# Kernel optimization log

Hardware: AMD Instinct MI355X
Metric: run time of the kernel (lower is better)

Reference implementation:

```python
import jax, jax.numpy as jnp
import numpy as np

DIM = 128
HEADS = 4
GN_GROUPS = 4
EPS = 1e-5


def setup_inputs() -> dict:
    key = jax.random.key(0)
    ks = jax.random.split(key, 6)
    B, C, H, W = 4, DIM, 64, 64
    x = jax.random.normal(ks[0], (B, C, H, W), dtype=jnp.float32)
    # 1x1 convs are channel matmuls: store as [out_ch, in_ch]
    w_qkv = jax.random.normal(ks[1], (3 * C, C), dtype=jnp.float32) * (C ** -0.5)
    w_out = jax.random.normal(ks[2], (C, C), dtype=jnp.float32) * (C ** -0.5)
    b_out = jax.random.normal(ks[3], (C,), dtype=jnp.float32) * 0.01
    gn_gamma = jnp.ones((C,), dtype=jnp.float32)
    gn_beta = jnp.zeros((C,), dtype=jnp.float32)
    return {"x": x, "w_qkv": w_qkv, "w_out": w_out, "b_out": b_out,
            "gn_gamma": gn_gamma, "gn_beta": gn_beta}


def _attention_block(x, w_qkv, w_out, b_out, gn_gamma, gn_beta):
    b, c, h, w = x.shape
    d = c // HEADS
    scale = d ** -0.5
    # 1x1 conv == per-pixel matmul over channels
    qkv = jnp.einsum('bchw,oc->bohw', x, w_qkv)  # [b, 3c, h, w]
    q, k, v = jnp.split(qkv, 3, axis=1)
    # 'b (h d) x y -> b h (x y) d'
    def to_heads(t):
        return t.reshape(b, HEADS, d, h * w).transpose(0, 1, 3, 2)  # [b, H, N, d]
    q, k, v = to_heads(q), to_heads(k), to_heads(v)
    dots = jnp.einsum('bhnd,bhmd->bhnm', q, k) * scale  # [b, H, N, N]
    attn = jax.nn.softmax(dots, axis=-1)
    out = jnp.einsum('bhnm,bhmd->bhnd', attn, v)  # [b, H, N, d]
    # 'b h (x y) d -> b (h d) x y'
    out = out.transpose(0, 1, 3, 2).reshape(b, c, h, w)
    # output 1x1 conv + bias
    out = jnp.einsum('bchw,oc->bohw', out, w_out) + b_out[None, :, None, None]
    # GroupNorm(4, c)
    g = out.reshape(b, GN_GROUPS, c // GN_GROUPS, h, w)
    mean = g.mean(axis=(2, 3, 4), keepdims=True)
    var = g.var(axis=(2, 3, 4), keepdims=True)
    g = (g - mean) * jax.lax.rsqrt(var + EPS)
    out = g.reshape(b, c, h, w) * gn_gamma[None, :, None, None] + gn_beta[None, :, None, None]
    return out + x


def reference(x, w_qkv, w_out, b_out, gn_gamma, gn_beta):
    return _attention_block(x, w_qkv, w_out, b_out, gn_gamma, gn_beta)
```

## Files before the change

kernel.cpp:

```cpp
#include <hip/hip_runtime.h>

#define DIM   128
#define NPIX  4096
#define DHEAD 32

using u16 = unsigned short;
typedef __attribute__((ext_vector_type(8))) short   short8;
typedef __attribute__((ext_vector_type(8))) u16     ushort8;
typedef __attribute__((ext_vector_type(4))) float   floatx4;
typedef __attribute__((ext_vector_type(2))) unsigned int uint2v;

#define SCL 0.25513899f

__device__ __forceinline__ float bf2f(u16 u) {
  union { unsigned int i; float f; } v; v.i = ((unsigned int)u) << 16; return v.f;
}
__device__ __forceinline__ u16 f2bf(float f) {
  union { unsigned int i; float f; } v; v.f = f;
  unsigned int i = v.i;
  return (u16)((i + 0x7FFFu + ((i >> 16) & 1u)) >> 16);
}
__device__ __forceinline__ unsigned int pk2bf(float a, float b) {
  union { float f; unsigned int u; } ua, ub; ua.f = a; ub.f = b;
  return __builtin_amdgcn_perm(ub.u, ua.u, 0x07060302u);
}

template<bool F32> __device__ __forceinline__ float ld1(const void* p, size_t i) {
  if constexpr (F32) return ((const float*)p)[i];
  else               return bf2f(((const u16*)p)[i]);
}
template<bool F32> __device__ __forceinline__ float4 ld4(const void* p, size_t i) {
  if constexpr (F32) {
    return *(const float4*)((const float*)p + i);
  } else {
    const ushort4 u = *(const ushort4*)((const u16*)p + i);
    return make_float4(bf2f(u.x), bf2f(u.y), bf2f(u.z), bf2f(u.w));
  }
}
template<bool F32> __device__ __forceinline__ void st4(void* p, size_t i, float4 v) {
  if constexpr (F32) {
    *(float4*)((float*)p + i) = v;
  } else {
    ushort4 u; u.x = f2bf(v.x); u.y = f2bf(v.y); u.z = f2bf(v.z); u.w = f2bf(v.w);
    *(ushort4*)((u16*)p + i) = u;
  }
}

__global__ void k_detect(const u16* __restrict__ x, int* __restrict__ flag,
                         float* __restrict__ S) {
  if (threadIdx.x < 40) S[threadIdx.x] = 0.f;
  if (threadIdx.x == 0 && blockIdx.x == 0) {
    int big = 0;
    for (int i = 0; i < 128; ++i) {
      const float v = bf2f(x[i]);
      if (!(fabsf(v) < 1e4f)) big = 1;
    }
    *flag = big;
  }
}

template<bool F32>
__global__ __launch_bounds__(256) void k_qkv(const void* __restrict__ x,
                                             const void* __restrict__ wqkv,
                                             u16* __restrict__ Q,
                                             u16* __restrict__ K,
                                             u16* __restrict__ V,
                                             const int* __restrict__ flag) {
  if (*flag != (F32 ? 1 : 0)) return;
  const int b = blockIdx.z, y = blockIdx.y, pt = blockIdx.x;
  const int tl = threadIdx.x;
  __shared__ float Ws[32 * 129];
  if (y < 8) {
    const int m = y >> 2, h = y & 3;
    const int ddq = tl & 3, pw = tl >> 2;
    const int rb = m * DIM + h * 32;
    for (int i = tl; i < 32 * DIM; i += 256)
      Ws[(i >> 7) * 129 + (i & 127)] =
          ld1<F32>(wqkv, (size_t)(rb + (i >> 7)) * DIM + (i & 127));
    __syncthreads();
    const int p0 = pt * 256 + pw * 4;
    float acc[8][4];
#pragma unroll
    for (int j = 0; j < 8; ++j) { acc[j][0] = acc[j][1] = acc[j][2] = acc[j][3] = 0.f; }
    const size_t xb = (size_t)b * DIM * NPIX + p0;
    for (int c = 0; c < DIM; ++c) {
      const float4 xv = ld4<F32>(x, xb + (size_t)c * NPIX);
#pragma unroll
      for (int j = 0; j < 8; ++j) {
        const float wv = Ws[(ddq * 8 + j) * 129 + c];
        acc[j][0] += wv * xv.x; acc[j][1] += wv * xv.y;
        acc[j][2] += wv * xv.z; acc[j][3] += wv * xv.w;
      }
    }
    u16* dst = (m == 0) ? Q : K;
    const float scl = (m == 0) ? 1.f : SCL;
    const int bh = b * 4 + h;
#pragma unroll
    for (int t = 0; t < 4; ++t) {
      ushort8 w8;
#pragma unroll
      for (int j = 0; j < 8; ++j) w8[j] = f2bf(acc[j][t] * scl);
      *(ushort8*)(dst + ((size_t)bh * NPIX + p0 + t) * DHEAD + ddq * 8) = w8;
    }
  } else {
    const int og = (y - 8) * 4 + (pt >> 2);
    const int ptv = pt & 3;
    for (int i = tl; i < 8 * DIM; i += 256)
      Ws[(i >> 7) * 129 + (i & 127)] =
          ld1<F32>(wqkv, (size_t)(2 * DIM + og * 8 + (i >> 7)) * DIM + (i & 127));
    __syncthreads();
    const int p0 = ptv * 1024 + tl * 4;
    float acc[8][4];
#pragma unroll
    for (int j = 0; j < 8; ++j) { acc[j][0] = acc[j][1] = acc[j][2] = acc[j][3] = 0.f; }
    const size_t xb = (size_t)b * DIM * NPIX + p0;
    for (int c = 0; c < DIM; ++c) {
      const float4 xv = ld4<F32>(x, xb + (size_t)c * NPIX);
#pragma unroll
      for (int j = 0; j < 8; ++j) {
        const float wv = Ws[j * 129 + c];
        acc[j][0] += wv * xv.x; acc[j][1] += wv * xv.y;
        acc[j][2] += wv * xv.z; acc[j][3] += wv * xv.w;
      }
    }
#pragma unroll
    for (int j = 0; j < 8; ++j) {
      const int c = og * 8 + j;
      ushort4 w4;
      w4.x = f2bf(acc[j][0]); w4.y = f2bf(acc[j][1]);
      w4.z = f2bf(acc[j][2]); w4.w = f2bf(acc[j][3]);
      *(ushort4*)(V + ((size_t)b * DIM + c) * NPIX + p0) = w4;
    }
  }
}

__device__ __forceinline__ short8 xform_p(unsigned c0, unsigned c1,
                                          unsigned c2, unsigned c3) {
  uint2v sw = __builtin_amdgcn_permlane32_swap(c0, c2, false, false);
  uint2v sx = __builtin_amdgcn_permlane16_swap(sw[0], sw[1], false, false);
  uint2v sy = __builtin_amdgcn_permlane32_swap(c1, c3, false, false);
  uint2v sz = __builtin_amdgcn_permlane16_swap(sy[0], sy[1], false, false);
  union { unsigned u[4]; short8 s; } r;
  r.u[0] = sx[0]; r.u[1] = sz[0]; r.u[2] = sx[1]; r.u[3] = sz[1];
  return r.s;
}

__global__ __launch_bounds__(256) void k_attn(const u16* __restrict__ Q,
                                              const u16* __restrict__ K,
                                              const u16* __restrict__ V,
                                              u16* __restrict__ O) {
  const int bh = blockIdx.y, qb = blockIdx.x;
  const int tid = threadIdx.x;
  const int wv = tid >> 6, lane = tid & 63;
  const int quad = lane >> 4, l15 = lane & 15;
  const int b = bh >> 2, h = bh & 3;

  __shared__ __align__(16) u16 Klds[2][64 * 40];
  __shared__ __align__(16) u16 Vlds[2][32 * 72];
  __shared__ __align__(16) u16 Olds[32 * 136];

  const int qtok0 = qb * 128 + wv * 32 + l15;
  const short8 qf0 = *(const short8*)(Q + ((size_t)bh * NPIX + qtok0) * DHEAD + quad * 8);
  const short8 qf1 = *(const short8*)(Q + ((size_t)bh * NPIX + qtok0 + 16) * DHEAD + quad * 8);

  floatx4 o00 = {0.f, 0.f, 0.f, 0.f}, o01 = {0.f, 0.f, 0.f, 0.f};
  floatx4 o10 = {0.f, 0.f, 0.f, 0.f}, o11 = {0.f, 0.f, 0.f, 0.f};
  float lp0 = 0.f, lp1 = 0.f;

  const int skey = tid >> 2, sqt = tid & 3;
  const int sdd = tid >> 3, soc = tid & 7;
  const u16* Kg = K + ((size_t)bh * NPIX + skey) * DHEAD + sqt * 8;
  const u16* Vg = V + ((size_t)(b * DIM + h * DHEAD + sdd)) * NPIX + soc * 8;

  {
    const ushort8 k0 = *(const ushort8*)Kg;
    const ushort8 v0 = *(const ushort8*)Vg;
    *(ushort8*)(Klds[0] + skey * 40 + sqt * 8) = k0;
    *(ushort8*)(Vlds[0] + sdd * 72 + soc * 8) = v0;
  }

  for (int ch = 0; ch < 64; ++ch) {
    const int cur = ch & 1, nxt = cur ^ 1;
    __syncthreads();
    ushort8 kpre, vpre;
    if (ch + 1 < 64) {
      kpre = *(const ushort8*)(Kg + (size_t)(ch + 1) * 64 * DHEAD);
      vpre = *(const ushort8*)(Vg + (ch + 1) * 64);
    }
#pragma unroll
    for (int kc = 0; kc < 2; ++kc) {
      unsigned ca[4], cb[4];
#pragma unroll
      for (int s = 0; s < 2; ++s) {
        const int sub = kc * 2 + s;
        const short8 af = *(const short8*)(Klds[cur] + (sub * 16 + l15) * 40 + quad * 8);
        const floatx4 s0 = __builtin_amdgcn_mfma_f32_16x16x32_bf16(
            af, qf0, (floatx4){0.f, 0.f, 0.f, 0.f}, 0, 0, 0);
        const floatx4 s1 = __builtin_amdgcn_mfma_f32_16x16x32_bf16(
            af, qf1, (floatx4){0.f, 0.f, 0.f, 0.f}, 0, 0, 0);
        const float a0 = __builtin_amdgcn_exp2f(s0[0]);
        const float a1 = __builtin_amdgcn_exp2f(s0[1]);
        const float a2 = __builtin_amdgcn_exp2f(s0[2]);
        const float a3 = __builtin_amdgcn_exp2f(s0[3]);
        const float b0 = __builtin_amdgcn_exp2f(s1[0]);
        const float b1 = __builtin_amdgcn_exp2f(s1[1]);
        const float b2 = __builtin_amdgcn_exp2f(s1[2]);
        const float b3 = __builtin_amdgcn_exp2f(s1[3]);
        lp0 += (a0 + a1) + (a2 + a3);
        lp1 += (b0 + b1) + (b2 + b3);
        ca[s * 2 + 0] = pk2bf(a0, a1); ca[s * 2 + 1] = pk2bf(a2, a3);
        cb[s * 2 + 0] = pk2bf(b0, b1); cb[s * 2 + 1] = pk2bf(b2, b3);
      }
      const short8 pa0 = xform_p(ca[0], ca[1], ca[2], ca[3]);
      const short8 pa1 = xform_p(cb[0], cb[1], cb[2], cb[3]);
      const short8 vb0 = *(const short8*)(Vlds[cur] + l15 * 72 + kc * 32 + quad * 8);
      const short8 vb1 = *(const short8*)(Vlds[cur] + (16 + l15) * 72 + kc * 32 + quad * 8);
      o00 = __builtin_amdgcn_mfma_f32_16x16x32_bf16(pa0, vb0, o00, 0, 0, 0);
      o01 = __builtin_amdgcn_mfma_f32_16x16x32_bf16(pa0, vb1, o01, 0, 0, 0);
      o10 = __builtin_amdgcn_mfma_f32_16x16x32_bf16(pa1, vb0, o10, 0, 0, 0);
      o11 = __builtin_amdgcn_mfma_f32_16x16x32_bf16(pa1, vb1, o11, 0, 0, 0);
    }
    if (ch + 1 < 64) {
      *(ushort8*)(Klds[nxt] + skey * 40 + sqt * 8) = kpre;
      *(ushort8*)(Vlds[nxt] + sdd * 72 + soc * 8) = vpre;
    }
  }
  float l0 = lp0, l1 = lp1;
  l0 += __shfl_xor(l0, 16); l0 += __shfl_xor(l0, 32);
  l1 += __shfl_xor(l1, 16); l1 += __shfl_xor(l1, 32);
  float li0[4], li1[4];
#pragma unroll
  for (int r = 0; r < 4; ++r) {
    li0[r] = 1.f / __shfl(l0, (lane & 48) | (quad * 4 + r));
    li1[r] = 1.f / __shfl(l1, (lane & 48) | (quad * 4 + r));
  }
  uint2v w00, w01, w10, w11;
  w00[0] = (unsigned)f2bf(o00[0] * li0[0]) | ((unsigned)f2bf(o00[1] * li0[1]) << 16);
  w00[1] = (unsigned)f2bf(o00[2] * li0[2]) | ((unsigned)f2bf(o00[3] * li0[3]) << 16);
  w01[0] = (unsigned)f2bf(o01[0] * li0[0]) | ((unsigned)f2bf(o01[1] * li0[1]) << 16);
  w01[1] = (unsigned)f2bf(o01[2] * li0[2]) | ((unsigned)f2bf(o01[3] * li0[3]) << 16);
  w10[0] = (unsigned)f2bf(o10[0] * li1[0]) | ((unsigned)f2bf(o10[1] * li1[1]) << 16);
  w10[1] = (unsigned)f2bf(o10[2] * li1[2]) | ((unsigned)f2bf(o10[3] * li1[3]) << 16);
  w11[0] = (unsigned)f2bf(o11[0] * li1[0]) | ((unsigned)f2bf(o11[1] * li1[1]) << 16);
  w11[1] = (unsigned)f2bf(o11[2] * li1[2]) | ((unsigned)f2bf(o11[3] * li1[3]) << 16);
  __syncthreads();
  *(uint2v*)(Olds + l15 * 136 + wv * 32 + quad * 4) = w00;
  *(uint2v*)(Olds + (16 + l15) * 136 + wv * 32 + quad * 4) = w01;
  *(uint2v*)(Olds + l15 * 136 + wv * 32 + 16 + quad * 4) = w10;
  *(uint2v*)(Olds + (16 + l15) * 136 + wv * 32 + 16 + quad * 4) = w11;
  __syncthreads();
  const int d = tid >> 3, oc = tid & 7;
  const u16* orow = Olds + d * 136;
  u16* og = O + ((size_t)(b * DIM + h * DHEAD + d)) * NPIX + qb * 128;
  *(ushort8*)(og + oc * 8)      = *(const ushort8*)(orow + oc * 8);
  *(ushort8*)(og + 64 + oc * 8) = *(const ushort8*)(orow + 64 + oc * 8);
}

template<bool F32>
__global__ __launch_bounds__(256) void k_proj(const u16* __restrict__ O,
                                              const void* __restrict__ wout,
                                              const void* __restrict__ bout,
                                              float* __restrict__ Y,
                                              float* __restrict__ Sred,
                                              const int* __restrict__ flag) {
  if (*flag != (F32 ? 1 : 0)) return;
  const int b = blockIdx.z, og = blockIdx.y, pt = blockIdx.x;
  const int tl = threadIdx.x;
  __shared__ float Ws[8][DIM];
  for (int i = tl; i < 8 * DIM; i += 256)
    Ws[i >> 7][i & 127] = ld1<F32>(wout, (size_t)(og * 8 + (i >> 7)) * DIM + (i & 127));
  __syncthreads();
  const int p0 = pt * 1024 + tl * 4;
  float acc[8][4];
#pragma unroll
  for (int j = 0; j < 8; ++j) { acc[j][0] = acc[j][1] = acc[j][2] = acc[j][3] = 0.f; }
  const u16* Ob = O + (size_t)b * DIM * NPIX + p0;
  for (int c = 0; c < DIM; ++c) {
    const ushort4 xv4 = *(const ushort4*)(Ob + (size_t)c * NPIX);
    const float x0 = bf2f(xv4.x), x1 = bf2f(xv4.y), x2 = bf2f(xv4.z), x3 = bf2f(xv4.w);
#pragma unroll
    for (int j = 0; j < 8; ++j) {
      const float wv = Ws[j][c];
      acc[j][0] += wv * x0; acc[j][1] += wv * x1;
      acc[j][2] += wv * x2; acc[j][3] += wv * x3;
    }
  }
  float s1 = 0.f, s2 = 0.f;
#pragma unroll
  for (int j = 0; j < 8; ++j) {
    const int o = og * 8 + j;
    const float bo = ld1<F32>(bout, o);
    float4 y4;
    y4.x = acc[j][0] + bo; y4.y = acc[j][1] + bo;
    y4.z = acc[j][2] + bo; y4.w = acc[j][3] + bo;
    *(float4*)(Y + ((size_t)b * DIM + o) * NPIX + p0) = y4;
    s1 += y4.x + y4.y + y4.z + y4.w;
    s2 += y4.x * y4.x + y4.y * y4.y + y4.z * y4.z + y4.w * y4.w;
  }
  __shared__ float red[2][256];
  red[0][tl] = s1; red[1][tl] = s2;
  __syncthreads();
  for (int off = 128; off >= 1; off >>= 1) {
    if (tl < off) { red[0][tl] += red[0][tl + off]; red[1][tl] += red[1][tl + off]; }
    __syncthreads();
  }
  if (tl == 0) {
    const int g = og >> 2;
    atomicAdd(&Sred[(b * 4 + g) * 2 + 0], red[0][0]);
    atomicAdd(&Sred[(b * 4 + g) * 2 + 1], red[1][0]);
  }
}

template<bool F32>
__global__ __launch_bounds__(256) void k_gn(const float* __restrict__ Y,
                                            const float* __restrict__ Sred,
                                            const void* __restrict__ x,
                                            const void* __restrict__ gamma,
                                            const void* __restrict__ beta,
                                            void* __restrict__ out,
                                            const int* __restrict__ flag) {
  if (*flag != (F32 ? 1 : 0)) return;
  const int idx = (blockIdx.x * 256 + threadIdx.x) * 4;
  const int b = idx >> 19;
  const int c = (idx >> 12) & 127;
  const int g = c >> 5;
  const float inv_n = 1.f / (32.f * 4096.f);
  const float s1 = Sred[(b * 4 + g) * 2 + 0];
  const float s2 = Sred[(b * 4 + g) * 2 + 1];
  const float mean = s1 * inv_n;
  const float var = s2 * inv_n - mean * mean;
  const float rs = rsqrtf(var + 1e-5f);
  const float ga = ld1<F32>(gamma, c) * rs;
  const float be = ld1<F32>(beta, c) - mean * ga;
  const float4 y4 = *(const float4*)(Y + idx);
  const float4 xv = ld4<F32>(x, idx);
  float4 r;
  r.x = y4.x * ga + be + xv.x;
  r.y = y4.y * ga + be + xv.y;
  r.z = y4.z * ga + be + xv.z;
  r.w = y4.w * ga + be + xv.w;
  st4<F32>(out, idx, r);
}

extern "C" void kernel_launch(void* const* d_in, const int* in_sizes, int n_in,
                              void* d_out, int out_size, void* d_ws, size_t ws_size,
                              hipStream_t stream) {
  const void* x     = d_in[0];
  const void* wqkv  = d_in[1];
  const void* wout  = d_in[2];
  const void* bout  = d_in[3];
  const void* gamma = d_in[4];
  const void* beta  = d_in[5];
  char* ws = (char*)d_ws;
  u16*   Q = (u16*)(ws + ((size_t)0  << 20));
  u16*   K = (u16*)(ws + ((size_t)8  << 20));
  u16*   V = (u16*)(ws + ((size_t)16 << 20));
  u16*   O = (u16*)(ws + ((size_t)24 << 20));
  float* Y = (float*)(ws + ((size_t)32 << 20));
  float* S = (float*)(ws + ((size_t)40 << 20));
  int*   F = (int*)(ws + ((size_t)40 << 20) + 128);

  k_detect<<<1, 64, 0, stream>>>((const u16*)x, F, S);

  k_qkv<false><<<dim3(16, 12, 4), 256, 0, stream>>>(x, wqkv, Q, K, V, F);
  k_qkv<true> <<<dim3(16, 12, 4), 256, 0, stream>>>(x, wqkv, Q, K, V, F);
  k_attn<<<dim3(32, 16), 256, 0, stream>>>(Q, K, V, O);
  k_proj<false><<<dim3(4, 16, 4), 256, 0, stream>>>(O, wout, bout, Y, S, F);
  k_proj<true> <<<dim3(4, 16, 4), 256, 0, stream>>>(O, wout, bout, Y, S, F);
  k_gn<false><<<2048, 256, 0, stream>>>(Y, S, x, gamma, beta, d_out, F);
  k_gn<true> <<<2048, 256, 0, stream>>>(Y, S, x, gamma, beta, d_out, F);
}
```

Measured before the change: 197.4 us.

## Split attention block across eight waves with 16 query rows each

The attention kernel now launches 512 threads per block, and each wave handles 16 query tokens instead of 32, so eight waves cover the same 128-query tile. K and V tile loads are split between the two halves of the block: the first 256 threads load K and the rest load V, each prefetching one vector per chunk. Per-wave register use and MFMA work are halved, which aims to raise occupancy and latency hiding on the 512-block grid. In exchange there are more waves sharing each LDS tile, barriers that span eight waves, and less reuse of each K fragment across queries.

```diff
diff --git a/kernel.cpp b/kernel.cpp
--- a/kernel.cpp
+++ b/kernel.cpp
@@ -145,7 +145,7 @@
   return r.s;
 }
 
-__global__ __launch_bounds__(256) void k_attn(const u16* __restrict__ Q,
+__global__ __launch_bounds__(512) void k_attn(const u16* __restrict__ Q,
                                               const u16* __restrict__ K,
                                               const u16* __restrict__ V,
                                               u16* __restrict__ O) {
@@ -159,101 +159,76 @@
   __shared__ __align__(16) u16 Vlds[2][32 * 72];
   __shared__ __align__(16) u16 Olds[32 * 136];
 
-  const int qtok0 = qb * 128 + wv * 32 + l15;
-  const short8 qf0 = *(const short8*)(Q + ((size_t)bh * NPIX + qtok0) * DHEAD + quad * 8);
-  const short8 qf1 = *(const short8*)(Q + ((size_t)bh * NPIX + qtok0 + 16) * DHEAD + quad * 8);
+  const int qtok0 = qb * 128 + wv * 16 + l15;
+  const short8 qf = *(const short8*)(Q + ((size_t)bh * NPIX + qtok0) * DHEAD + quad * 8);
 
   floatx4 o00 = {0.f, 0.f, 0.f, 0.f}, o01 = {0.f, 0.f, 0.f, 0.f};
-  floatx4 o10 = {0.f, 0.f, 0.f, 0.f}, o11 = {0.f, 0.f, 0.f, 0.f};
-  float lp0 = 0.f, lp1 = 0.f;
-
-  const int skey = tid >> 2, sqt = tid & 3;
-  const int sdd = tid >> 3, soc = tid & 7;
-  const u16* Kg = K + ((size_t)bh * NPIX + skey) * DHEAD + sqt * 8;
-  const u16* Vg = V + ((size_t)(b * DIM + h * DHEAD + sdd)) * NPIX + soc * 8;
-
-  {
-    const ushort8 k0 = *(const ushort8*)Kg;
-    const ushort8 v0 = *(const ushort8*)Vg;
-    *(ushort8*)(Klds[0] + skey * 40 + sqt * 8) = k0;
-    *(ushort8*)(Vlds[0] + sdd * 72 + soc * 8) = v0;
-  }
+  float lp0 = 0.f;
+
+  const int st = tid & 255;
+  const bool isK = tid < 256;
+  const int skey = st >> 2, sqt = st & 3;
+  const int sdd = st >> 3, soc = st & 7;
+  const u16* Gg = isK ? (K + ((size_t)bh * NPIX + skey) * DHEAD + sqt * 8)
+                      : (V + ((size_t)(b * DIM + h * DHEAD + sdd)) * NPIX + soc * 8);
+  u16* Ld0 = isK ? (Klds[0] + skey * 40 + sqt * 8) : (Vlds[0] + sdd * 72 + soc * 8);
+  u16* Ld1 = isK ? (Klds[1] + skey * 40 + sqt * 8) : (Vlds[1] + sdd * 72 + soc * 8);
+  const size_t gstride = isK ? (size_t)(64 * DHEAD) : (size_t)64;
+
+  *(ushort8*)Ld0 = *(const ushort8*)Gg;
 
   for (int ch = 0; ch < 64; ++ch) {
-    const int cur = ch & 1, nxt = cur ^ 1;
+    const int cur = ch & 1;
     __syncthreads();
-    ushort8 kpre, vpre;
+    ushort8 pre;
     if (ch + 1 < 64) {
-      kpre = *(const ushort8*)(Kg + (size_t)(ch + 1) * 64 * DHEAD);
-      vpre = *(const ushort8*)(Vg + (ch + 1) * 64);
+      pre = *(const ushort8*)(Gg + (size_t)(ch + 1) * gstride);
     }
 #pragma unroll
     for (int kc = 0; kc < 2; ++kc) {
-      unsigned ca[4], cb[4];
+      unsigned ca[4];
 #pragma unroll
       for (int s = 0; s < 2; ++s) {
         const int sub = kc * 2 + s;
         const short8 af = *(const short8*)(Klds[cur] + (sub * 16 + l15) * 40 + quad * 8);
         const floatx4 s0 = __builtin_amdgcn_mfma_f32_16x16x32_bf16(
-            af, qf0, (floatx4){0.f, 0.f, 0.f, 0.f}, 0, 0, 0);
-        const floatx4 s1 = __builtin_amdgcn_mfma_f32_16x16x32_bf16(
-            af, qf1, (floatx4){0.f, 0.f, 0.f, 0.f}, 0, 0, 0);
+            af, qf, (floatx4){0.f, 0.f, 0.f, 0.f}, 0, 0, 0);
         const float a0 = __builtin_amdgcn_exp2f(s0[0]);
         const float a1 = __builtin_amdgcn_exp2f(s0[1]);
         const float a2 = __builtin_amdgcn_exp2f(s0[2]);
         const float a3 = __builtin_amdgcn_exp2f(s0[3]);
-        const float b0 = __builtin_amdgcn_exp2f(s1[0]);
-        const float b1 = __builtin_amdgcn_exp2f(s1[1]);
-        const float b2 = __builtin_amdgcn_exp2f(s1[2]);
-        const float b3 = __builtin_amdgcn_exp2f(s1[3]);
         lp0 += (a0 + a1) + (a2 + a3);
-        lp1 += (b0 + b1) + (b2 + b3);
         ca[s * 2 + 0] = pk2bf(a0, a1); ca[s * 2 + 1] = pk2bf(a2, a3);
-        cb[s * 2 + 0] = pk2bf(b0, b1); cb[s * 2 + 1] = pk2bf(b2, b3);
       }
-      const short8 pa0 = xform_p(ca[0], ca[1], ca[2], ca[3]);
-      const short8 pa1 = xform_p(cb[0], cb[1], cb[2], cb[3]);
+      const short8 pa = xform_p(ca[0], ca[1], ca[2], ca[3]);
       const short8 vb0 = *(const short8*)(Vlds[cur] + l15 * 72 + kc * 32 + quad * 8);
       const short8 vb1 = *(const short8*)(Vlds[cur] + (16 + l15) * 72 + kc * 32 + quad * 8);
-      o00 = __builtin_amdgcn_mfma_f32_16x16x32_bf16(pa0, vb0, o00, 0, 0, 0);
-      o01 = __builtin_amdgcn_mfma_f32_16x16x32_bf16(pa0, vb1, o01, 0, 0, 0);
-      o10 = __builtin_amdgcn_mfma_f32_16x16x32_bf16(pa1, vb0, o10, 0, 0, 0);
-      o11 = __builtin_amdgcn_mfma_f32_16x16x32_bf16(pa1, vb1, o11, 0, 0, 0);
+      o00 = __builtin_amdgcn_mfma_f32_16x16x32_bf16(pa, vb0, o00, 0, 0, 0);
+      o01 = __builtin_amdgcn_mfma_f32_16x16x32_bf16(pa, vb1, o01, 0, 0, 0);
     }
     if (ch + 1 < 64) {
-      *(ushort8*)(Klds[nxt] + skey * 40 + sqt * 8) = kpre;
-      *(ushort8*)(Vlds[nxt] + sdd * 72 + soc * 8) = vpre;
-    }
-  }
-  float l0 = lp0, l1 = lp1;
+      *(ushort8*)(cur ? Ld0 : Ld1) = pre;
+    }
+  }
+  float l0 = lp0;
   l0 += __shfl_xor(l0, 16); l0 += __shfl_xor(l0, 32);
-  l1 += __shfl_xor(l1, 16); l1 += __shfl_xor(l1, 32);
-  float li0[4], li1[4];
+  float li[4];
 #pragma unroll
   for (int r = 0; r < 4; ++r) {
-    li0[r] = 1.f / __shfl(l0, (lane & 48) | (quad * 4 + r));
-    li1[r] = 1.f / __shfl(l1, (lane & 48) | (quad * 4 + r));
-  }
-  uint2v w00, w01, w10, w11;
-  w00[0] = (unsigned)f2bf(o00[0] * li0[0]) | ((unsigned)f2bf(o00[1] * li0[1]) << 16);
-  w00[1] = (unsigned)f2bf(o00[2] * li0[2]) | ((unsigned)f2bf(o00[3] * li0[3]) << 16);
-  w01[0] = (unsigned)f2bf(o01[0] * li0[0]) | ((unsigned)f2bf(o01[1] * li0[1]) << 16);
-  w01[1] = (unsigned)f2bf(o01[2] * li0[2]) | ((unsigned)f2bf(o01[3] * li0[3]) << 16);
-  w10[0] = (unsigned)f2bf(o10[0] * li1[0]) | ((unsigned)f2bf(o10[1] * li1[1]) << 16);
-  w10[1] = (unsigned)f2bf(o10[2] * li1[2]) | ((unsigned)f2bf(o10[3] * li1[3]) << 16);
-  w11[0] = (unsigned)f2bf(o11[0] * li1[0]) | ((unsigned)f2bf(o11[1] * li1[1]) << 16);
-  w11[1] = (unsigned)f2bf(o11[2] * li1[2]) | ((unsigned)f2bf(o11[3] * li1[3]) << 16);
+    li[r] = 1.f / __shfl(l0, (lane & 48) | (quad * 4 + r));
+  }
+  uint2v w00, w01;
+  w00[0] = (unsigned)f2bf(o00[0] * li[0]) | ((unsigned)f2bf(o00[1] * li[1]) << 16);
+  w00[1] = (unsigned)f2bf(o00[2] * li[2]) | ((unsigned)f2bf(o00[3] * li[3]) << 16);
+  w01[0] = (unsigned)f2bf(o01[0] * li[0]) | ((unsigned)f2bf(o01[1] * li[1]) << 16);
+  w01[1] = (unsigned)f2bf(o01[2] * li[2]) | ((unsigned)f2bf(o01[3] * li[3]) << 16);
   __syncthreads();
-  *(uint2v*)(Olds + l15 * 136 + wv * 32 + quad * 4) = w00;
-  *(uint2v*)(Olds + (16 + l15) * 136 + wv * 32 + quad * 4) = w01;
-  *(uint2v*)(Olds + l15 * 136 + wv * 32 + 16 + quad * 4) = w10;
-  *(uint2v*)(Olds + (16 + l15) * 136 + wv * 32 + 16 + quad * 4) = w11;
+  *(uint2v*)(Olds + l15 * 136 + wv * 16 + quad * 4) = w00;
+  *(uint2v*)(Olds + (16 + l15) * 136 + wv * 16 + quad * 4) = w01;
   __syncthreads();
-  const int d = tid >> 3, oc = tid & 7;
-  const u16* orow = Olds + d * 136;
+  const int d = tid >> 4, oc = tid & 15;
   u16* og = O + ((size_t)(b * DIM + h * DHEAD + d)) * NPIX + qb * 128;
-  *(ushort8*)(og + oc * 8)      = *(const ushort8*)(orow + oc * 8);
-  *(ushort8*)(og + 64 + oc * 8) = *(const ushort8*)(orow + 64 + oc * 8);
+  *(ushort8*)(og + oc * 8) = *(const ushort8*)(Olds + d * 136 + oc * 8);
 }
 
 template<bool F32>
@@ -364,7 +339,7 @@
 
   k_qkv<false><<<dim3(16, 12, 4), 256, 0, stream>>>(x, wqkv, Q, K, V, F);
   k_qkv<true> <<<dim3(16, 12, 4), 256, 0, stream>>>(x, wqkv, Q, K, V, F);
-  k_attn<<<dim3(32, 16), 256, 0, stream>>>(Q, K, V, O);
+  k_attn<<<dim3(32, 16), 512, 0, stream>>>(Q, K, V, O);
   k_proj<false><<<dim3(4, 16, 4), 256, 0, stream>>>(O, wout, bout, Y, S, F);
   k_proj<true> <<<dim3(4, 16, 4), 256, 0, stream>>>(O, wout, bout, Y, S, F);
   k_gn<false><<<2048, 256, 0, stream>>>(Y, S, x, gamma, beta, d_out, F);
```

Result: faster. 190.5 us (-3.5%).
